# Kernel tuning notes

Hardware: AMD Instinct MI355X
Metric: run time of the kernel (lower is better)

## Reference

```python
import jax, jax.numpy as jnp
import numpy as np

B, I, J, C = 1, 320, 320, 128
H, Dh = 4, 32
AH = H * Dh  # all_head_size == 128
EPS = 1e-5


def setup_inputs() -> dict:
    key = jax.random.key(0)
    ks = jax.random.split(key, 10)
    s = 0.05
    return {
        "z": jax.random.normal(ks[0], (B, I, J, C), jnp.float32),
        "z_mask": jax.random.randint(ks[1], (B, I, J), 0, 2, jnp.int32),
        "ln_scale": jnp.ones((C,), jnp.float32),
        "ln_bias": jnp.zeros((C,), jnp.float32),
        "Wq": jax.random.normal(ks[2], (C, AH), jnp.float32) * s,
        "Wk": jax.random.normal(ks[3], (C, AH), jnp.float32) * s,
        "Wv": jax.random.normal(ks[4], (C, AH), jnp.float32) * s,
        "Wg": jax.random.normal(ks[5], (C, AH), jnp.float32) * s,
        "bg": jnp.zeros((AH,), jnp.float32),
        "Wo": jax.random.normal(ks[6], (AH, C), jnp.float32) * s,
        "bo": jnp.zeros((C,), jnp.float32),
    }


def _layernorm(x, scale, bias):
    mu = jnp.mean(x, axis=-1, keepdims=True)
    var = jnp.var(x, axis=-1, keepdims=True)
    return (x - mu) * jax.lax.rsqrt(var + EPS) * scale + bias


def reference(z, z_mask, ln_scale, ln_bias, Wq, Wk, Wv, Wg, bg, Wo, bo):
    zn = _layernorm(z, ln_scale, ln_bias)                  # [B,I,J,C]
    m = z_mask.astype(jnp.float32)                         # [B,I,J]
    mask_bias = 1e9 * (m - 1.0)[:, :, None, None, :]       # [B,I,1,1,J]

    def heads(x):
        return x.reshape(x.shape[:-1] + (H, Dh))

    q = heads(zn @ Wq)                                     # [B,I,J,H,Dh]
    k = heads(zn @ Wk)
    v = heads(zn @ Wv)
    # NOTE: original module applies NO 1/sqrt(d) scaling — faithful.
    logits = jnp.einsum('biqhc,bikhc->bihqk', q, k) + mask_bias
    weights = jax.nn.softmax(logits, axis=-1)              # [B,I,H,J,J]
    wa = jnp.einsum('bihqk,bikhc->biqhc', weights, v)      # [B,I,J,H,Dh]
    g = jax.nn.sigmoid(heads(zn @ Wg + bg))                # [B,I,J,H,Dh]
    out = (g * wa).reshape(z.shape[:-1] + (AH,))           # [B,I,J,AH]
    return (out @ Wo + bo) * m[..., None]                  # [B,I,J,C]
```

## Files before the change

kernel.cpp:

```cpp
#include <hip/hip_runtime.h>

typedef _Float16 f16;
typedef _Float16 f16x2 __attribute__((ext_vector_type(2)));
typedef _Float16 f16x4 __attribute__((ext_vector_type(4)));
typedef _Float16 f16x8 __attribute__((ext_vector_type(8)));
typedef float f32x4 __attribute__((ext_vector_type(4)));

#define I_DIM 320
#define J_DIM 320
#define C_DIM 128
#define NROWS (I_DIM * J_DIM)
#define LOG2E 1.44269504f

__device__ inline float pkrtz(float a, float b) {
    return __builtin_bit_cast(float, __builtin_amdgcn_cvt_pkrtz(a, b));
}

__global__ __launch_bounds__(256) void prep_kernel(const float* __restrict__ Wq,
                                                   const float* __restrict__ Wk,
                                                   const float* __restrict__ Wv,
                                                   const float* __restrict__ Wg,
                                                   const float* __restrict__ Wo,
                                                   f16* __restrict__ Wfrag) {
    int f = blockIdx.x * 256 + threadIdx.x;
    int j = f & 7, lane = (f >> 3) & 63, n = (f >> 9) & 7;
    int ks = (f >> 12) & 3, w = f >> 14;
    int gq = lane >> 4, r16 = lane & 15;
    const float* W = (w == 0) ? Wq : (w == 1) ? Wk : (w == 2) ? Wv : (w == 3) ? Wg : Wo;
    Wfrag[f] = (f16)W[(size_t)(ks * 32 + gq * 8 + j) * 128 + n * 16 + r16];
}

__global__ __launch_bounds__(256) void ln_kernel(const float* __restrict__ z,
                                                 const float* __restrict__ scale,
                                                 const float* __restrict__ bias,
                                                 f16* __restrict__ zn) {
    int wave = threadIdx.x >> 6;
    int lane = threadIdx.x & 63;
    int row = blockIdx.x * 4 + wave;
    const float* zr = z + (size_t)row * C_DIM;
    float2 x = *(const float2*)(zr + lane * 2);
    float s = x.x + x.y;
    float sq = x.x * x.x + x.y * x.y;
    #pragma unroll
    for (int o = 32; o; o >>= 1) {
        s  += __shfl_xor(s, o);
        sq += __shfl_xor(sq, o);
    }
    float mu = s * (1.0f / 128.0f);
    float var = sq * (1.0f / 128.0f) - mu * mu;
    float rs = rsqrtf(var + 1e-5f);
    int c0 = lane * 2;
    float y0 = (x.x - mu) * rs * scale[c0] + bias[c0];
    float y1 = (x.y - mu) * rs * scale[c0 + 1] + bias[c0 + 1];
    f16x2 o2 = {(f16)y0, (f16)y1};
    *(f16x2*)(zn + (size_t)row * C_DIM + c0) = o2;
}

__global__ __launch_bounds__(256, 3) void attn_mega(const f16* __restrict__ zn,
                                                    const f16* __restrict__ Wfrag,
                                                    const float* __restrict__ bg,
                                                    const int* __restrict__ z_mask,
                                                    f16* __restrict__ gwa) {
    __shared__ f16 Ksh[320][40];
    __shared__ f16 Vt[32][328];
    __shared__ f16 mbs[320];
    __shared__ f16 Pb[4][16][40];

    int bid = blockIdx.x;
    int xcd = bid & 7, idx = bid >> 3;
    int i = xcd * 40 + (idx >> 2);
    int h = idx & 3;
    size_t zbase = (size_t)i * (J_DIM * C_DIM);
    size_t gbase = zbase + h * 32;

    int wave = threadIdx.x >> 6;
    int lane = threadIdx.x & 63;
    int gq = lane >> 4, r16 = lane & 15;

    const f16* wfq = Wfrag;
    const f16* wfk = Wfrag + 16384;
    const f16* wfv = Wfrag + 32768;
    const f16* wfg = Wfrag + 49152;

    for (int t = threadIdx.x; t < 320; t += 256)
        mbs[t] = (f16)(z_mask[i * J_DIM + t] ? -12.0f : -60000.0f);

    for (int rt = wave; rt < 20; rt += 4) {
        f16x8 a[4];
        #pragma unroll
        for (int ks = 0; ks < 4; ++ks)
            a[ks] = *(const f16x8*)(zn + zbase + (size_t)(rt * 16 + r16) * C_DIM + ks * 32 + gq * 8);
        f32x4 kacc[2] = {}, vacc[2] = {};
        #pragma unroll
        for (int ks = 0; ks < 4; ++ks) {
            #pragma unroll
            for (int n = 0; n < 2; ++n) {
                f16x8 bk = *(const f16x8*)(wfk + (ks * 8 + 2 * h + n) * 512 + lane * 8);
                kacc[n] = __builtin_amdgcn_mfma_f32_16x16x32_f16(a[ks], bk, kacc[n], 0, 0, 0);
                f16x8 bv = *(const f16x8*)(wfv + (ks * 8 + 2 * h + n) * 512 + lane * 8);
                vacc[n] = __builtin_amdgcn_mfma_f32_16x16x32_f16(a[ks], bv, vacc[n], 0, 0, 0);
            }
        }
        int colbase = (rt >> 1) * 32 + gq * 8 + (rt & 1) * 4;
        #pragma unroll
        for (int n = 0; n < 2; ++n) {
            #pragma unroll
            for (int rr = 0; rr < 4; ++rr)
                Ksh[rt * 16 + gq * 4 + rr][n * 16 + r16] = (f16)kacc[n][rr];
            f16x4 vp = {(f16)vacc[n][0], (f16)vacc[n][1], (f16)vacc[n][2], (f16)vacc[n][3]};
            *(f16x4*)(&Vt[n * 16 + r16][colbase]) = vp;
        }
    }
    __syncthreads();

    f16x8 qa[5];
    #pragma unroll
    for (int u = 0; u < 5; ++u) {
        int qt = u * 4 + wave;
        f16x8 a[4];
        #pragma unroll
        for (int ks = 0; ks < 4; ++ks)
            a[ks] = *(const f16x8*)(zn + zbase + (size_t)(qt * 16 + r16) * C_DIM + ks * 32 + gq * 8);
        f32x4 qacc[2] = {};
        #pragma unroll
        for (int ks = 0; ks < 4; ++ks) {
            #pragma unroll
            for (int n = 0; n < 2; ++n) {
                f16x8 bq = *(const f16x8*)(wfq + (ks * 8 + 2 * h + n) * 512 + lane * 8);
                qacc[n] = __builtin_amdgcn_mfma_f32_16x16x32_f16(a[ks], bq, qacc[n], 0, 0, 0);
            }
        }
        #pragma unroll
        for (int n = 0; n < 2; ++n)
            #pragma unroll
            for (int rr = 0; rr < 4; ++rr)
                Pb[wave][gq * 4 + rr][n * 16 + r16] = (f16)qacc[n][rr];
        asm volatile("s_waitcnt lgkmcnt(0)" ::: "memory");
        qa[u] = *(const f16x8*)(&Pb[wave][r16][gq * 8]);
    }

    const f32x4 zero = {};
    f32x4 wa[5][2] = {};
    float s[5] = {0.f, 0.f, 0.f, 0.f, 0.f};

    for (int kc = 0; kc < 10; ++kc) {
        f16x8 kb0 = *(const f16x8*)(&Ksh[kc * 32 + r16][gq * 8]);
        f16x8 kb1 = *(const f16x8*)(&Ksh[kc * 32 + 16 + r16][gq * 8]);
        f16x4 mk0 = *(const f16x4*)(&mbs[kc * 32 + 4 * gq]);
        f16x4 mk1 = *(const f16x4*)(&mbs[kc * 32 + 16 + 4 * gq]);
        f16x8 vb0 = *(const f16x8*)(&Vt[r16][kc * 32 + gq * 8]);
        f16x8 vb1 = *(const f16x8*)(&Vt[16 + r16][kc * 32 + gq * 8]);
        #pragma unroll
        for (int u = 0; u < 5; ++u) {
            f32x4 sc0 = __builtin_amdgcn_mfma_f32_16x16x32_f16(kb0, qa[u], zero, 0, 0, 0);
            f32x4 sc1 = __builtin_amdgcn_mfma_f32_16x16x32_f16(kb1, qa[u], zero, 0, 0, 0);
            float p0[4], p1[4];
            #pragma unroll
            for (int r = 0; r < 4; ++r) {
                p0[r] = __builtin_amdgcn_exp2f(fminf(fmaf(sc0[r], LOG2E, (float)mk0[r]), 15.0f));
                p1[r] = __builtin_amdgcn_exp2f(fminf(fmaf(sc1[r], LOG2E, (float)mk1[r]), 15.0f));
                s[u] += p0[r] + p1[r];
            }
            union { float f[4]; f16x8 v; } pu;
            pu.f[0] = pkrtz(p0[0], p0[1]);
            pu.f[1] = pkrtz(p0[2], p0[3]);
            pu.f[2] = pkrtz(p1[0], p1[1]);
            pu.f[3] = pkrtz(p1[2], p1[3]);
            wa[u][0] = __builtin_amdgcn_mfma_f32_16x16x32_f16(pu.v, vb0, wa[u][0], 0, 0, 0);
            wa[u][1] = __builtin_amdgcn_mfma_f32_16x16x32_f16(pu.v, vb1, wa[u][1], 0, 0, 0);
        }
    }

    float bgv0 = bg[h * 32 + r16];
    float bgv1 = bg[h * 32 + 16 + r16];
    #pragma unroll
    for (int u = 0; u < 5; ++u) {
        int qt = u * 4 + wave;
        float su = s[u];
        su += __shfl_xor(su, 16);
        su += __shfl_xor(su, 32);
        float rinv[4];
        #pragma unroll
        for (int r = 0; r < 4; ++r)
            rinv[r] = 1.0f / __shfl(su, gq * 4 + r);
        f16x8 a[4];
        #pragma unroll
        for (int ks = 0; ks < 4; ++ks)
            a[ks] = *(const f16x8*)(zn + zbase + (size_t)(qt * 16 + r16) * C_DIM + ks * 32 + gq * 8);
        f32x4 gacc[2] = {};
        #pragma unroll
        for (int ks = 0; ks < 4; ++ks) {
            #pragma unroll
            for (int n = 0; n < 2; ++n) {
                f16x8 bgf = *(const f16x8*)(wfg + (ks * 8 + 2 * h + n) * 512 + lane * 8);
                gacc[n] = __builtin_amdgcn_mfma_f32_16x16x32_f16(a[ks], bgf, gacc[n], 0, 0, 0);
            }
        }
        #pragma unroll
        for (int n = 0; n < 2; ++n) {
            float bgn = n ? bgv1 : bgv0;
            #pragma unroll
            for (int r = 0; r < 4; ++r) {
                int jq = qt * 16 + gq * 4 + r;
                int dh = n * 16 + r16;
                float gv = 1.0f / (1.0f + __expf(-(gacc[n][r] + bgn)));
                gwa[gbase + (size_t)jq * C_DIM + dh] = (f16)(gv * wa[u][n][r] * rinv[r]);
            }
        }
    }
}

__global__ __launch_bounds__(256) void out_kernel(const f16* __restrict__ gwa,
                                                  const f16* __restrict__ Wofrag,
                                                  const float* __restrict__ bo,
                                                  const int* __restrict__ z_mask,
                                                  float* __restrict__ out) {
    int wave = threadIdx.x >> 6;
    int lane = threadIdx.x & 63;
    int gq = lane >> 4, r16 = lane & 15;
    int row0 = blockIdx.x * 256 + wave * 64;

    f32x4 acc[4][8] = {};
    #pragma unroll
    for (int ks = 0; ks < 4; ++ks) {
        f16x8 a[4];
        #pragma unroll
        for (int m = 0; m < 4; ++m)
            a[m] = *(const f16x8*)(gwa + (size_t)(row0 + m * 16 + r16) * C_DIM + ks * 32 + gq * 8);
        #pragma unroll
        for (int n = 0; n < 8; ++n) {
            f16x8 b = *(const f16x8*)(Wofrag + (ks * 8 + n) * 512 + lane * 8);
            #pragma unroll
            for (int m = 0; m < 4; ++m)
                acc[m][n] = __builtin_amdgcn_mfma_f32_16x16x32_f16(a[m], b, acc[m][n], 0, 0, 0);
        }
    }
    #pragma unroll
    for (int m = 0; m < 4; ++m) {
        #pragma unroll
        for (int rr = 0; rr < 4; ++rr) {
            int row = row0 + m * 16 + gq * 4 + rr;
            float mk = (float)z_mask[row];
            #pragma unroll
            for (int n = 0; n < 8; ++n) {
                int col = n * 16 + r16;
                out[(size_t)row * C_DIM + col] = (acc[m][n][rr] + bo[col]) * mk;
            }
        }
    }
}

extern "C" void kernel_launch(void* const* d_in, const int* in_sizes, int n_in,
                              void* d_out, int out_size, void* d_ws, size_t ws_size,
                              hipStream_t stream) {
    const float* z        = (const float*)d_in[0];
    const int*   z_mask   = (const int*)d_in[1];
    const float* ln_scale = (const float*)d_in[2];
    const float* ln_bias  = (const float*)d_in[3];
    const float* Wq       = (const float*)d_in[4];
    const float* Wk       = (const float*)d_in[5];
    const float* Wv       = (const float*)d_in[6];
    const float* Wg       = (const float*)d_in[7];
    const float* bg       = (const float*)d_in[8];
    const float* Wo       = (const float*)d_in[9];
    const float* bo       = (const float*)d_in[10];
    float* out = (float*)d_out;

    char* ws = (char*)d_ws;
    const size_t SZ = (size_t)NROWS * C_DIM * sizeof(f16);
    f16* zn    = (f16*)(ws);
    f16* gwa   = (f16*)(ws + 1 * SZ);
    f16* Wfrag = (f16*)(ws + 2 * SZ);

    prep_kernel<<<320, 256, 0, stream>>>(Wq, Wk, Wv, Wg, Wo, Wfrag);
    ln_kernel  <<<NROWS / 4, 256, 0, stream>>>(z, ln_scale, ln_bias, zn);
    attn_mega  <<<I_DIM * 4, 256, 0, stream>>>(zn, Wfrag, bg, z_mask, gwa);
    out_kernel <<<NROWS / 256, 256, 0, stream>>>(gwa, Wfrag + 4 * 16384, bo, z_mask, out);
}
```

Baseline: 109.1 us.

## Fold log2e into Wq, inject mask via MFMA accumulator, compute row sums with MFMA

Pre-scales the Q weights by log2(e) so scores come out of the MFMA already in base-2, and seeds the score MFMA accumulator with the fp32 mask bias, which removes the per-element fma, min-clamp and f16-to-f32 convert before exp2. The softmax denominator is now an extra MFMA of P against a ones vector rather than scalar adds plus cross-lane shuffles. The upper clamp at 15 is dropped, so large logits could overflow the f16 P values. The extra MFMA per tile also adds matrix-core work to the inner loop.

Result: no change. 110.0 us (+0.8%).

```diff
diff --git a/kernel.cpp b/kernel.cpp
--- a/kernel.cpp
+++ b/kernel.cpp
@@ -27,7 +27,9 @@
     int ks = (f >> 12) & 3, w = f >> 14;
     int gq = lane >> 4, r16 = lane & 15;
     const float* W = (w == 0) ? Wq : (w == 1) ? Wk : (w == 2) ? Wv : (w == 3) ? Wg : Wo;
-    Wfrag[f] = (f16)W[(size_t)(ks * 32 + gq * 8 + j) * 128 + n * 16 + r16];
+    float val = W[(size_t)(ks * 32 + gq * 8 + j) * 128 + n * 16 + r16];
+    if (w == 0) val *= LOG2E;
+    Wfrag[f] = (f16)val;
 }
 
 __global__ __launch_bounds__(256) void ln_kernel(const float* __restrict__ z,
@@ -63,7 +65,7 @@
                                                     f16* __restrict__ gwa) {
     __shared__ f16 Ksh[320][40];
     __shared__ f16 Vt[32][328];
-    __shared__ f16 mbs[320];
+    __shared__ float mbs[320];
     __shared__ f16 Pb[4][16][40];
 
     int bid = blockIdx.x;
@@ -83,7 +85,7 @@
     const f16* wfg = Wfrag + 49152;
 
     for (int t = threadIdx.x; t < 320; t += 256)
-        mbs[t] = (f16)(z_mask[i * J_DIM + t] ? -12.0f : -60000.0f);
+        mbs[t] = z_mask[i * J_DIM + t] ? -12.0f : -60000.0f;
 
     for (int rt = wave; rt < 20; rt += 4) {
         f16x8 a[4];
@@ -139,27 +141,26 @@
         qa[u] = *(const f16x8*)(&Pb[wave][r16][gq * 8]);
     }
 
-    const f32x4 zero = {};
+    const f16x8 ones = {(f16)1, (f16)1, (f16)1, (f16)1, (f16)1, (f16)1, (f16)1, (f16)1};
     f32x4 wa[5][2] = {};
-    float s[5] = {0.f, 0.f, 0.f, 0.f, 0.f};
+    f32x4 wa2[5] = {};
 
     for (int kc = 0; kc < 10; ++kc) {
         f16x8 kb0 = *(const f16x8*)(&Ksh[kc * 32 + r16][gq * 8]);
         f16x8 kb1 = *(const f16x8*)(&Ksh[kc * 32 + 16 + r16][gq * 8]);
-        f16x4 mk0 = *(const f16x4*)(&mbs[kc * 32 + 4 * gq]);
-        f16x4 mk1 = *(const f16x4*)(&mbs[kc * 32 + 16 + 4 * gq]);
+        f32x4 mk0 = *(const f32x4*)(&mbs[kc * 32 + 4 * gq]);
+        f32x4 mk1 = *(const f32x4*)(&mbs[kc * 32 + 16 + 4 * gq]);
         f16x8 vb0 = *(const f16x8*)(&Vt[r16][kc * 32 + gq * 8]);
         f16x8 vb1 = *(const f16x8*)(&Vt[16 + r16][kc * 32 + gq * 8]);
         #pragma unroll
         for (int u = 0; u < 5; ++u) {
-            f32x4 sc0 = __builtin_amdgcn_mfma_f32_16x16x32_f16(kb0, qa[u], zero, 0, 0, 0);
-            f32x4 sc1 = __builtin_amdgcn_mfma_f32_16x16x32_f16(kb1, qa[u], zero, 0, 0, 0);
+            f32x4 sc0 = __builtin_amdgcn_mfma_f32_16x16x32_f16(kb0, qa[u], mk0, 0, 0, 0);
+            f32x4 sc1 = __builtin_amdgcn_mfma_f32_16x16x32_f16(kb1, qa[u], mk1, 0, 0, 0);
             float p0[4], p1[4];
             #pragma unroll
             for (int r = 0; r < 4; ++r) {
-                p0[r] = __builtin_amdgcn_exp2f(fminf(fmaf(sc0[r], LOG2E, (float)mk0[r]), 15.0f));
-                p1[r] = __builtin_amdgcn_exp2f(fminf(fmaf(sc1[r], LOG2E, (float)mk1[r]), 15.0f));
-                s[u] += p0[r] + p1[r];
+                p0[r] = __builtin_amdgcn_exp2f(sc0[r]);
+                p1[r] = __builtin_amdgcn_exp2f(sc1[r]);
             }
             union { float f[4]; f16x8 v; } pu;
             pu.f[0] = pkrtz(p0[0], p0[1]);
@@ -168,6 +169,7 @@
             pu.f[3] = pkrtz(p1[2], p1[3]);
             wa[u][0] = __builtin_amdgcn_mfma_f32_16x16x32_f16(pu.v, vb0, wa[u][0], 0, 0, 0);
             wa[u][1] = __builtin_amdgcn_mfma_f32_16x16x32_f16(pu.v, vb1, wa[u][1], 0, 0, 0);
+            wa2[u]   = __builtin_amdgcn_mfma_f32_16x16x32_f16(pu.v, ones, wa2[u], 0, 0, 0);
         }
     }
 
@@ -176,13 +178,10 @@
     #pragma unroll
     for (int u = 0; u < 5; ++u) {
         int qt = u * 4 + wave;
-        float su = s[u];
-        su += __shfl_xor(su, 16);
-        su += __shfl_xor(su, 32);
         float rinv[4];
         #pragma unroll
         for (int r = 0; r < 4; ++r)
-            rinv[r] = 1.0f / __shfl(su, gq * 4 + r);
+            rinv[r] = 1.0f / wa2[u][r];
         f16x8 a[4];
         #pragma unroll
         for (int ks = 0; ks < 4; ++ks)
```
